# Kernel tuning notes

Measured on AMD Instinct MI355X. Metric: run time of the kernel, lower is better.

## Reference

```python
import jax, jax.numpy as jnp
import numpy as np

N_NODES = 1000000
N_EDGES = 32000000
NUM_GRAPHS = 1024


def setup_inputs() -> dict:
    key = jax.random.key(0)
    k1, k2, k3, k4, k5 = jax.random.split(key, 5)
    x = jax.random.normal(k1, (N_NODES, 1), dtype=jnp.float32)
    W = jax.random.normal(k2, (1, 1), dtype=jnp.float32)
    b = jax.random.normal(k3, (1,), dtype=jnp.float32)
    edge_index = jax.random.randint(k4, (2, N_EDGES), 0, N_NODES, dtype=jnp.int64)
    batch = jnp.sort(jax.random.randint(k5, (N_NODES,), 0, NUM_GRAPHS, dtype=jnp.int64))
    return {"x": x, "W": W, "b": b, "edge_index": edge_index, "batch": batch}


def reference(x, W, b, edge_index, batch):
    src, dst = edge_index[0], edge_index[1]
    # SimpleConv (default sum aggregation): out[i] = sum_{(j->i) in E} x[j]
    agg = jax.ops.segment_sum(x[src], dst, num_segments=N_NODES)  # [N,1]
    h = jax.nn.relu(agg)
    # global_mean_pool over graph ids
    sums = jax.ops.segment_sum(h, batch, num_segments=NUM_GRAPHS)  # [G,1]
    counts = jax.ops.segment_sum(jnp.ones((N_NODES,), dtype=h.dtype), batch,
                                 num_segments=NUM_GRAPHS)  # [G]
    pooled = sums / jnp.maximum(counts, 1.0)[:, None]
    # Linear(1 -> 1): y = pooled @ W^T + b
    return pooled @ W.T + b
```

## Files before the change

kernel.cpp:

```cpp
#include <hip/hip_runtime.h>

#define N_NODES    1000000
#define N_EDGES    32000000
#define NUM_GRAPHS 1024

typedef int          vint4  __attribute__((ext_vector_type(4)));
typedef unsigned int uint32;
typedef unsigned int vuint4 __attribute__((ext_vector_type(4)));

#define BUCKET_SHIFT 12
#define BUCKET_NODES (1 << BUCKET_SHIFT)
#define NBUCKETS     245

#define T1_NCHUNK   512
#define T1_BLOCK    512
#define T1_EDGES_PER_CHUNK (N_EDGES / T1_NCHUNK)
#define T1_QUADS    (T1_EDGES_PER_CHUNK / 4)
#define T1_QPR      (2 * T1_BLOCK)
#define T1_ROUNDS   ((T1_QUADS + T1_QPR - 1) / T1_QPR)
#define SCAP        64
#define SLAB_CAP    368

#define RSPLIT        4
#define CELLS_PER_WG  (T1_NCHUNK / RSPLIT)

#define T2_CAP      136192
#define T2_NCHUNK   512
#define T2_EPC      (N_EDGES / T2_NCHUNK)

#define GLDS(gp, lp) __builtin_amdgcn_global_load_lds(                         \
    (const __attribute__((address_space(1))) void*)(gp),                       \
    (__attribute__((address_space(3))) void*)(lp), 4, 0, 0)

__global__ __launch_bounds__(T1_BLOCK)
void slab_scatter(const int* __restrict__ src,
                  const int* __restrict__ dst,
                  uint32* __restrict__ slab,
                  uint32* __restrict__ fcnt_g,
                  uint32* __restrict__ ecnt_g) {
    __shared__ uint32 stage[NBUCKETS][SCAP];
    __shared__ uint32 rpos[NBUCKETS];
    __shared__ uint32 ecnt[NBUCKETS];
    __shared__ uint32 flushed[NBUCKETS];
    __shared__ uint32 carry[NBUCKETS];

    const int tid = threadIdx.x;
    const int w   = blockIdx.x;
    const vint4* d4 = (const vint4*)(dst + (size_t)w * T1_EDGES_PER_CHUNK);
    const vint4* s4 = (const vint4*)(src + (size_t)w * T1_EDGES_PER_CHUNK);

    for (int b = tid; b < NBUCKETS; b += T1_BLOCK) {
        rpos[b] = 0; ecnt[b] = 0; flushed[b] = 0; carry[b] = 0;
    }
    __syncthreads();

    const int grp    = tid >> 4;
    const int lane16 = tid & 15;

    for (int r = 0; r < T1_ROUNDS; ++r) {
        const int q0 = r * T1_QPR + tid;
        const int q1 = q0 + T1_BLOCK;
        const bool ok0 = q0 < T1_QUADS;
        const bool ok1 = q1 < T1_QUADS;
        vint4 d0, s0, d1, s1;
        if (ok0) { d0 = __builtin_nontemporal_load(&d4[q0]);
                   s0 = __builtin_nontemporal_load(&s4[q0]); }
        if (ok1) { d1 = __builtin_nontemporal_load(&d4[q1]);
                   s1 = __builtin_nontemporal_load(&s4[q1]); }

#define SCAT4(dd4, ss4)                                                        \
        {                                                                      \
            _Pragma("unroll")                                                  \
            for (int k = 0; k < 4; ++k) {                                      \
                uint32 dd = (uint32)(k == 0 ? dd4.x : k == 1 ? dd4.y :         \
                                     k == 2 ? dd4.z : dd4.w);                  \
                uint32 ss = (uint32)(k == 0 ? ss4.x : k == 1 ? ss4.y :         \
                                     k == 2 ? ss4.z : ss4.w);                  \
                uint32 b  = dd >> BUCKET_SHIFT;                                \
                uint32 v  = ((dd & (BUCKET_NODES - 1)) << 20) | ss;            \
                uint32 c  = carry[b] + atomicAdd(&rpos[b], 1u);                \
                if (c < SCAP) {                                                \
                    stage[b][c] = v;                                           \
                } else {                                                       \
                    uint32 e = atomicAdd(&ecnt[b], 1u);                        \
                    if (e < SLAB_CAP)          \
                        __builtin_nontemporal_store(v,                         \
                            &slab[((size_t)b * T1_NCHUNK + w) * SLAB_CAP       \
                                  + (SLAB_CAP - 1 - e)]);                      \
                }                                                              \
            }                                                                  \
        }
        if (ok0) SCAT4(d0, s0)
        if (ok1) SCAT4(d1, s1)
#undef SCAT4
        __syncthreads();
        for (int b = grp; b < NBUCKETS; b += 32) {
            uint32 tot = carry[b] + rpos[b];
            if (tot > SCAP) tot = SCAP;
            uint32 lines = tot >> 4;
            uint32 rem   = tot & 15u;
            uint32 fl    = flushed[b];
            uint32 maxl  = (SLAB_CAP > fl) ? ((SLAB_CAP - fl) >> 4) : 0u;
            if (lines > maxl) lines = maxl;
            uint32* dp = slab + ((size_t)b * T1_NCHUNK + w) * SLAB_CAP + fl;
            for (uint32 l = 0; l < lines; ++l)
                __builtin_nontemporal_store(stage[b][l * 16 + lane16],
                                            &dp[l * 16 + lane16]);
            if (lines) {
                uint32 mv = 0;
                if (lane16 < rem) mv = stage[b][lines * 16 + lane16];
                if (lane16 < rem) stage[b][lane16] = mv;
            }
            if (lane16 == 0) {
                flushed[b] = fl + lines * 16;
                carry[b]   = rem;
                rpos[b]    = 0;
            }
        }
        __syncthreads();
    }
    for (int b = grp; b < NBUCKETS; b += 32) {
        uint32 rem = carry[b];
        uint32 fl  = flushed[b];
        uint32* dp = slab + ((size_t)b * T1_NCHUNK + w) * SLAB_CAP + fl;
        if (lane16 < rem && fl + lane16 < SLAB_CAP)
            __builtin_nontemporal_store(stage[b][lane16], &dp[lane16]);
        if (lane16 == 0) {
            uint32 fc = fl + rem;
            fcnt_g[(size_t)b * T1_NCHUNK + w] = fc > SLAB_CAP ? SLAB_CAP : fc;
            ecnt_g[(size_t)b * T1_NCHUNK + w] = ecnt[b];
        }
    }
}

__global__ __launch_bounds__(1024)
void slab_reduce2(const uint32* __restrict__ slab,
                  const uint32* __restrict__ fcnt_g,
                  const uint32* __restrict__ ecnt_g,
                  const float* __restrict__ x,
                  float* __restrict__ agg) {
    __shared__ float  acc[BUCKET_NODES];
    __shared__ float  scr[16][8][64];
    __shared__ uint32 fc_s[CELLS_PER_WG];
    __shared__ uint32 ec_s[CELLS_PER_WG];

    const int b    = blockIdx.x / RSPLIT;
    const int part = blockIdx.x % RSPLIT;
    const int tid  = threadIdx.x;

    for (int n = tid; n < BUCKET_NODES; n += 1024) acc[n] = 0.0f;
    if (tid < CELLS_PER_WG) {
        size_t cell = (size_t)b * T1_NCHUNK + (size_t)part * CELLS_PER_WG + tid;
        uint32 fc = fcnt_g[cell];
        uint32 ec = ecnt_g[cell];
        if (fc > SLAB_CAP) fc = SLAB_CAP;
        if (ec > SLAB_CAP) ec = SLAB_CAP;
        fc_s[tid] = fc;
        ec_s[tid] = ec;
    }
    __syncthreads();

    const int wv = tid >> 6, lane = tid & 63;
    const size_t cbase = (size_t)b * T1_NCHUNK + (size_t)part * CELLS_PER_WG;

    for (int cp = wv; cp < CELLS_PER_WG; cp += 32) {
        const int cA = cp, cB = cp + 16;
        const uint32 fcA = fc_s[cA], fcB = fc_s[cB];
        const uint32 ecA = ec_s[cA], ecB = ec_s[cB];
        const uint32* baseA = slab + (cbase + cA) * SLAB_CAP;
        const uint32* baseB = slab + (cbase + cB) * SLAB_CAP;
        const uint32 nqA = fcA >> 2, nqB = fcB >> 2;
        const uint32 nqM = nqA > nqB ? nqA : nqB;

        for (uint32 i = lane; i < nqM; i += 64) {
            const bool aOK = i < nqA, bOK = i < nqB;
            vuint4 va = {0, 0, 0, 0}, vb = {0, 0, 0, 0};
            if (aOK) va = __builtin_nontemporal_load(&((const vuint4*)baseA)[i]);
            if (bOK) vb = __builtin_nontemporal_load(&((const vuint4*)baseB)[i]);
            GLDS(x + (va.x & 0xFFFFFu), &scr[wv][0][0]);
            GLDS(x + (va.y & 0xFFFFFu), &scr[wv][1][0]);
            GLDS(x + (va.z & 0xFFFFFu), &scr[wv][2][0]);
            GLDS(x + (va.w & 0xFFFFFu), &scr[wv][3][0]);
            GLDS(x + (vb.x & 0xFFFFFu), &scr[wv][4][0]);
            GLDS(x + (vb.y & 0xFFFFFu), &scr[wv][5][0]);
            GLDS(x + (vb.z & 0xFFFFFu), &scr[wv][6][0]);
            GLDS(x + (vb.w & 0xFFFFFu), &scr[wv][7][0]);
            asm volatile("s_waitcnt vmcnt(0)" ::: "memory");
            __builtin_amdgcn_sched_barrier(0);
            float a0 = scr[wv][0][lane], a1 = scr[wv][1][lane];
            float a2 = scr[wv][2][lane], a3 = scr[wv][3][lane];
            float b0 = scr[wv][4][lane], b1 = scr[wv][5][lane];
            float b2 = scr[wv][6][lane], b3 = scr[wv][7][lane];
            if (aOK) { atomicAdd(&acc[va.x >> 20], a0); atomicAdd(&acc[va.y >> 20], a1);
                       atomicAdd(&acc[va.z >> 20], a2); atomicAdd(&acc[va.w >> 20], a3); }
            if (bOK) { atomicAdd(&acc[vb.x >> 20], b0); atomicAdd(&acc[vb.y >> 20], b1);
                       atomicAdd(&acc[vb.z >> 20], b2); atomicAdd(&acc[vb.w >> 20], b3); }
            __builtin_amdgcn_sched_barrier(0);
        }
#define REM(base, fc, ec)                                                      \
        {                                                                      \
            for (uint32 i = ((fc) & ~3u) + lane; i < (fc); i += 64) {          \
                uint32 v = __builtin_nontemporal_load(&(base)[i]);             \
                atomicAdd(&acc[v >> 20], x[v & 0xFFFFFu]);                     \
            }                                                                  \
            for (uint32 i = lane; i < (ec); i += 64) {                         \
                uint32 v = (base)[SLAB_CAP - 1 - i];                           \
                atomicAdd(&acc[v >> 20], x[v & 0xFFFFFu]);                     \
            }                                                                  \
        }
        REM(baseA, fcA, ecA)
        REM(baseB, fcB, ecB)
#undef REM
    }
    __syncthreads();

    const int node0 = b << BUCKET_SHIFT;
    for (int n = tid; n < BUCKET_NODES; n += 1024) {
        float v = acc[n];
        if (v != 0.0f) atomicAdd(&agg[node0 + n], v);
    }
}

__global__ void finalize_kernel(const float* __restrict__ sums,
                                const float* __restrict__ counts,
                                const float* __restrict__ W,
                                const float* __restrict__ b,
                                float* __restrict__ out) {
    int g = blockIdx.x * blockDim.x + threadIdx.x;
    if (g < NUM_GRAPHS) {
        float pooled = sums[g] / fmaxf(counts[g], 1.0f);
        out[g] = pooled * W[0] + b[0];
    }
}

__global__ __launch_bounds__(1024)
void bucket_scatter(const int* __restrict__ src,
                    const int* __restrict__ dst,
                    uint32* __restrict__ sorted,
                    uint32* __restrict__ gpos) {
    __shared__ uint32 hist[NBUCKETS];
    __shared__ uint32 pos[NBUCKETS];
    const int tid = threadIdx.x;
    const size_t base = (size_t)blockIdx.x * T2_EPC;
    for (int b = tid; b < NBUCKETS; b += 1024) hist[b] = 0;
    __syncthreads();
    const vint4* d4 = (const vint4*)(dst + base);
    const vint4* s4 = (const vint4*)(src + base);
    const int nvec = T2_EPC / 4;
    for (int i = tid; i < nvec; i += 1024) {
        vint4 d = d4[i];
        atomicAdd(&hist[(uint32)d.x >> BUCKET_SHIFT], 1u);
        atomicAdd(&hist[(uint32)d.y >> BUCKET_SHIFT], 1u);
        atomicAdd(&hist[(uint32)d.z >> BUCKET_SHIFT], 1u);
        atomicAdd(&hist[(uint32)d.w >> BUCKET_SHIFT], 1u);
    }
    __syncthreads();
    for (int b = tid; b < NBUCKETS; b += 1024)
        pos[b] = atomicAdd(&gpos[b], hist[b]);
    __syncthreads();
    for (int i = tid; i < nvec; i += 1024) {
        vint4 d = d4[i];
        vint4 s = s4[i];
        #pragma unroll
        for (int k = 0; k < 4; ++k) {
            uint32 dd = (uint32)(k == 0 ? d.x : k == 1 ? d.y : k == 2 ? d.z : d.w);
            uint32 ss = (uint32)(k == 0 ? s.x : k == 1 ? s.y : k == 2 ? s.z : s.w);
            uint32 b = dd >> BUCKET_SHIFT, dl = dd & (BUCKET_NODES - 1);
            uint32 slot = atomicAdd(&pos[b], 1u);
            if (slot < T2_CAP) sorted[(size_t)b * T2_CAP + slot] = (dl << 20) | ss;
        }
    }
}

__global__ __launch_bounds__(1024)
void bucket_reduce(const uint32* __restrict__ sorted,
                   const uint32* __restrict__ gpos,
                   const float* __restrict__ x,
                   const int* __restrict__ batch,
                   float* __restrict__ sums,
                   float* __restrict__ counts) {
    __shared__ float acc[BUCKET_NODES];
    const int b = blockIdx.x;
    const int tid = threadIdx.x;
    for (int n = tid; n < BUCKET_NODES; n += 1024) acc[n] = 0.0f;
    __syncthreads();
    uint32 cnt = gpos[b];
    if (cnt > T2_CAP) cnt = T2_CAP;
    const uint32* reg = sorted + (size_t)b * T2_CAP;
    const vuint4* r4 = (const vuint4*)reg;
    const uint32 nvec = cnt / 4;
    for (uint32 i = tid; i < nvec; i += 1024) {
        vuint4 v = r4[i];
        atomicAdd(&acc[v.x >> 20], x[v.x & 0xFFFFFu]);
        atomicAdd(&acc[v.y >> 20], x[v.y & 0xFFFFFu]);
        atomicAdd(&acc[v.z >> 20], x[v.z & 0xFFFFFu]);
        atomicAdd(&acc[v.w >> 20], x[v.w & 0xFFFFFu]);
    }
    for (uint32 i = nvec * 4 + tid; i < cnt; i += 1024) {
        uint32 v = reg[i];
        atomicAdd(&acc[v >> 20], x[v & 0xFFFFFu]);
    }
    __syncthreads();
    const int node0 = b << BUCKET_SHIFT;
    for (int n = tid; n < BUCKET_NODES; n += 1024) {
        int i = node0 + n;
        float h = 0.0f;
        int g = -1;
        if (i < N_NODES) {
            h = fmaxf(acc[n], 0.0f);
            g = batch[i];
        }
        int g0 = __shfl(g, 0);
        if (__all(g == g0)) {
            #pragma unroll
            for (int off = 32; off > 0; off >>= 1)
                h += __shfl_down(h, off);
            if ((tid & 63) == 0 && g0 >= 0) {
                atomicAdd(&sums[g0], h);
                atomicAdd(&counts[g0], 64.0f);
            }
        } else if (g >= 0) {
            atomicAdd(&sums[g], h);
            atomicAdd(&counts[g], 1.0f);
        }
    }
}

__global__ void scatter_edges_dev(const vint4* __restrict__ src4,
                                  const vint4* __restrict__ dst4,
                                  const float* __restrict__ x,
                                  float* __restrict__ agg) {
    int t = blockIdx.x * blockDim.x + threadIdx.x;
    if (t < N_EDGES / 4) {
        vint4 s = __builtin_nontemporal_load(&src4[t]);
        vint4 d = __builtin_nontemporal_load(&dst4[t]);
        atomicAdd(&agg[d.x], x[s.x]);
        atomicAdd(&agg[d.y], x[s.y]);
        atomicAdd(&agg[d.z], x[s.z]);
        atomicAdd(&agg[d.w], x[s.w]);
    }
}

__global__ void pool_nodes_kernel(const float* __restrict__ agg,
                                  const int* __restrict__ batch,
                                  float* __restrict__ sums,
                                  float* __restrict__ counts) {
    int i = blockIdx.x * blockDim.x + threadIdx.x;
    float h = 0.0f;
    int g = -1;
    if (i < N_NODES) {
        h = fmaxf(agg[i], 0.0f);
        g = batch[i];
    }
    int g0 = __shfl(g, 0);
    if (__all(g == g0)) {
        #pragma unroll
        for (int off = 32; off > 0; off >>= 1)
            h += __shfl_down(h, off);
        if ((threadIdx.x & 63) == 0 && g0 >= 0) {
            atomicAdd(&sums[g0], h);
            atomicAdd(&counts[g0], 64.0f);
        }
    } else if (g >= 0) {
        atomicAdd(&sums[g], h);
        atomicAdd(&counts[g], 1.0f);
    }
}

extern "C" void kernel_launch(void* const* d_in, const int* in_sizes, int n_in,
                              void* d_out, int out_size, void* d_ws, size_t ws_size,
                              hipStream_t stream) {
    const float* x     = (const float*)d_in[0];
    const float* W     = (const float*)d_in[1];
    const float* b     = (const float*)d_in[2];
    const int*   edge  = (const int*)d_in[3];
    const int*   batch = (const int*)d_in[4];
    float* out = (float*)d_out;

    const int* src = edge;
    const int* dst = edge + N_EDGES;

    const size_t ncells     = (size_t)NBUCKETS * T1_NCHUNK;
    const size_t slab_elems = ncells * SLAB_CAP;
    const size_t nagg       = (size_t)NBUCKETS * BUCKET_NODES;
    const size_t need0 = (slab_elems + 2 * ncells + nagg + 2 * NUM_GRAPHS) * 4;
    const size_t t2_elems = (size_t)NBUCKETS * T2_CAP;
    const size_t need2 = (t2_elems + 256 + 2 * NUM_GRAPHS) * 4;

    if (ws_size >= need0) {
        uint32* slab   = (uint32*)d_ws;
        uint32* fcnt_g = slab + slab_elems;
        uint32* ecnt_g = fcnt_g + ncells;
        float*  agg    = (float*)(ecnt_g + ncells);
        float*  sums   = agg + nagg;
        float*  counts = sums + NUM_GRAPHS;
        (void)hipMemsetAsync(agg, 0, (nagg + 2 * NUM_GRAPHS) * 4, stream);

        slab_scatter<<<T1_NCHUNK, T1_BLOCK, 0, stream>>>(src, dst, slab, fcnt_g, ecnt_g);
        slab_reduce2<<<NBUCKETS * RSPLIT, 1024, 0, stream>>>(slab, fcnt_g, ecnt_g, x, agg);
        pool_nodes_kernel<<<(N_NODES + 255) / 256, 256, 0, stream>>>(agg, batch, sums, counts);
        finalize_kernel<<<(NUM_GRAPHS + 255) / 256, 256, 0, stream>>>(sums, counts, W, b, out);
    } else if (ws_size >= need2) {
        uint32* sorted = (uint32*)d_ws;
        uint32* gpos   = sorted + t2_elems;
        float*  sums   = (float*)(gpos + 256);
        float*  counts = sums + NUM_GRAPHS;
        (void)hipMemsetAsync(gpos, 0, (256 + 2 * NUM_GRAPHS) * 4, stream);

        bucket_scatter<<<T2_NCHUNK, 1024, 0, stream>>>(src, dst, sorted, gpos);
        bucket_reduce<<<NBUCKETS, 1024, 0, stream>>>(sorted, gpos, x, batch, sums, counts);
        finalize_kernel<<<(NUM_GRAPHS + 255) / 256, 256, 0, stream>>>(sums, counts, W, b, out);
    } else {
        float* agg    = (float*)d_ws;
        float* sums   = agg + N_NODES;
        float* counts = sums + NUM_GRAPHS;
        (void)hipMemsetAsync(d_ws, 0, ((size_t)N_NODES + 2 * NUM_GRAPHS) * 4, stream);

        int nthreads = N_EDGES / 4;
        scatter_edges_dev<<<(nthreads + 255) / 256, 256, 0, stream>>>(
            (const vint4*)src, (const vint4*)dst, x, agg);
        pool_nodes_kernel<<<(N_NODES + 255) / 256, 256, 0, stream>>>(agg, batch, sums, counts);
        finalize_kernel<<<(NUM_GRAPHS + 255) / 256, 256, 0, stream>>>(sums, counts, W, b, out);
    }
}
```

Measured before the change: 644.1 us.

## Gather source features during scatter and store value plus 16-bit local destination

Adds a new scatter/reduce path. The scatter kernel reads x[src] for each edge up front and writes two slabs: a float value and a 16-bit bucket-local destination. The reduce kernel then accumulates those values straight into LDS without gathering x. This moves the random x gather into the streaming pass and avoids a second indirect lookup. In exchange each slab entry grows from 4 to 6 bytes, the LDS staging depth per bucket is halved (more edges spill to the scattered overflow path), and the path needs a larger workspace to be taken.

```diff
diff --git a/kernel.cpp b/kernel.cpp
--- a/kernel.cpp
+++ b/kernel.cpp
@@ -4,9 +4,11 @@
 #define N_EDGES    32000000
 #define NUM_GRAPHS 1024
 
-typedef int          vint4  __attribute__((ext_vector_type(4)));
-typedef unsigned int uint32;
-typedef unsigned int vuint4 __attribute__((ext_vector_type(4)));
+typedef int            vint4    __attribute__((ext_vector_type(4)));
+typedef unsigned int   uint32;
+typedef unsigned int   vuint4   __attribute__((ext_vector_type(4)));
+typedef unsigned short vushort4 __attribute__((ext_vector_type(4)));
+typedef float          vfloat4  __attribute__((ext_vector_type(4)));
 
 #define BUCKET_SHIFT 12
 #define BUCKET_NODES (1 << BUCKET_SHIFT)
@@ -19,6 +21,7 @@
 #define T1_QPR      (2 * T1_BLOCK)
 #define T1_ROUNDS   ((T1_QUADS + T1_QPR - 1) / T1_QPR)
 #define SCAP        64
+#define SCAP_V      32
 #define SLAB_CAP    368
 
 #define RSPLIT        4
@@ -31,6 +34,193 @@
 #define GLDS(gp, lp) __builtin_amdgcn_global_load_lds(                         \
     (const __attribute__((address_space(1))) void*)(gp),                       \
     (__attribute__((address_space(3))) void*)(lp), 4, 0, 0)
+
+__global__ __launch_bounds__(T1_BLOCK)
+void slab_scatter_v(const int* __restrict__ src,
+                    const int* __restrict__ dst,
+                    const float* __restrict__ x,
+                    float*  __restrict__ vslab,
+                    unsigned short* __restrict__ dslab,
+                    uint32* __restrict__ fcnt_g,
+                    uint32* __restrict__ ecnt_g) {
+    __shared__ float          stage_v[NBUCKETS][SCAP_V];
+    __shared__ unsigned short stage_d[NBUCKETS][SCAP_V];
+    __shared__ uint32 rpos[NBUCKETS];
+    __shared__ uint32 ecnt[NBUCKETS];
+    __shared__ uint32 flushed[NBUCKETS];
+    __shared__ uint32 carry[NBUCKETS];
+
+    const int tid = threadIdx.x;
+    const int w   = blockIdx.x;
+    const vint4* d4 = (const vint4*)(dst + (size_t)w * T1_EDGES_PER_CHUNK);
+    const vint4* s4 = (const vint4*)(src + (size_t)w * T1_EDGES_PER_CHUNK);
+
+    for (int b = tid; b < NBUCKETS; b += T1_BLOCK) {
+        rpos[b] = 0; ecnt[b] = 0; flushed[b] = 0; carry[b] = 0;
+    }
+    __syncthreads();
+
+    const int grp    = tid >> 4;
+    const int lane16 = tid & 15;
+
+    for (int r = 0; r < T1_ROUNDS; ++r) {
+        const int q0 = r * T1_QPR + tid;
+        const int q1 = q0 + T1_BLOCK;
+        const bool ok0 = q0 < T1_QUADS;
+        const bool ok1 = q1 < T1_QUADS;
+        vint4 d0, s0, d1, s1;
+        if (ok0) { d0 = __builtin_nontemporal_load(&d4[q0]);
+                   s0 = __builtin_nontemporal_load(&s4[q0]); }
+        if (ok1) { d1 = __builtin_nontemporal_load(&d4[q1]);
+                   s1 = __builtin_nontemporal_load(&s4[q1]); }
+
+        float fv[8];
+        uint32 dv[8];
+        #pragma unroll
+        for (int k = 0; k < 8; ++k) {
+            const bool ok = (k < 4) ? ok0 : ok1;
+            if (ok) {
+                uint32 dd, ss;
+                if (k < 4) {
+                    dd = (uint32)(k == 0 ? d0.x : k == 1 ? d0.y : k == 2 ? d0.z : d0.w);
+                    ss = (uint32)(k == 0 ? s0.x : k == 1 ? s0.y : k == 2 ? s0.z : s0.w);
+                } else {
+                    dd = (uint32)(k == 4 ? d1.x : k == 5 ? d1.y : k == 6 ? d1.z : d1.w);
+                    ss = (uint32)(k == 4 ? s1.x : k == 5 ? s1.y : k == 6 ? s1.z : s1.w);
+                }
+                dv[k] = dd;
+                fv[k] = x[ss];
+            }
+        }
+        #pragma unroll
+        for (int k = 0; k < 8; ++k) {
+            const bool ok = (k < 4) ? ok0 : ok1;
+            if (ok) {
+                uint32 dd = dv[k];
+                uint32 b  = dd >> BUCKET_SHIFT;
+                uint32 dl = dd & (BUCKET_NODES - 1);
+                uint32 c  = carry[b] + atomicAdd(&rpos[b], 1u);
+                if (c < SCAP_V) {
+                    stage_v[b][c] = fv[k];
+                    stage_d[b][c] = (unsigned short)dl;
+                } else {
+                    uint32 e = atomicAdd(&ecnt[b], 1u);
+                    if (e < SLAB_CAP) {
+                        size_t idx = ((size_t)b * T1_NCHUNK + w) * SLAB_CAP
+                                     + (SLAB_CAP - 1 - e);
+                        __builtin_nontemporal_store(fv[k], &vslab[idx]);
+                        __builtin_nontemporal_store((unsigned short)dl, &dslab[idx]);
+                    }
+                }
+            }
+        }
+        __syncthreads();
+        for (int b = grp; b < NBUCKETS; b += 32) {
+            uint32 tot = carry[b] + rpos[b];
+            if (tot > SCAP_V) tot = SCAP_V;
+            uint32 lines = tot >> 4;
+            uint32 rem   = tot & 15u;
+            uint32 fl    = flushed[b];
+            uint32 maxl  = (SLAB_CAP > fl) ? ((SLAB_CAP - fl) >> 4) : 0u;
+            if (lines > maxl) lines = maxl;
+            size_t cbase = ((size_t)b * T1_NCHUNK + w) * SLAB_CAP + fl;
+            for (uint32 l = 0; l < lines; ++l) {
+                __builtin_nontemporal_store(stage_v[b][l * 16 + lane16],
+                                            &vslab[cbase + l * 16 + lane16]);
+                __builtin_nontemporal_store(stage_d[b][l * 16 + lane16],
+                                            &dslab[cbase + l * 16 + lane16]);
+            }
+            if (lines) {
+                float  mv = 0.0f; unsigned short md = 0;
+                if (lane16 < rem) { mv = stage_v[b][lines * 16 + lane16];
+                                    md = stage_d[b][lines * 16 + lane16]; }
+                if (lane16 < rem) { stage_v[b][lane16] = mv;
+                                    stage_d[b][lane16] = md; }
+            }
+            if (lane16 == 0) {
+                flushed[b] = fl + lines * 16;
+                carry[b]   = rem;
+                rpos[b]    = 0;
+            }
+        }
+        __syncthreads();
+    }
+    for (int b = grp; b < NBUCKETS; b += 32) {
+        uint32 rem = carry[b];
+        uint32 fl  = flushed[b];
+        size_t cbase = ((size_t)b * T1_NCHUNK + w) * SLAB_CAP + fl;
+        if (lane16 < rem && fl + lane16 < SLAB_CAP) {
+            __builtin_nontemporal_store(stage_v[b][lane16], &vslab[cbase + lane16]);
+            __builtin_nontemporal_store(stage_d[b][lane16], &dslab[cbase + lane16]);
+        }
+        if (lane16 == 0) {
+            uint32 fc = fl + rem;
+            fcnt_g[(size_t)b * T1_NCHUNK + w] = fc > SLAB_CAP ? SLAB_CAP : fc;
+            ecnt_g[(size_t)b * T1_NCHUNK + w] = ecnt[b];
+        }
+    }
+}
+
+__global__ __launch_bounds__(1024)
+void slab_reduce_v(const float* __restrict__ vslab,
+                   const unsigned short* __restrict__ dslab,
+                   const uint32* __restrict__ fcnt_g,
+                   const uint32* __restrict__ ecnt_g,
+                   float* __restrict__ agg) {
+    __shared__ float  acc[BUCKET_NODES];
+    __shared__ uint32 fc_s[CELLS_PER_WG];
+    __shared__ uint32 ec_s[CELLS_PER_WG];
+
+    const int b    = blockIdx.x / RSPLIT;
+    const int part = blockIdx.x % RSPLIT;
+    const int tid  = threadIdx.x;
+
+    for (int n = tid; n < BUCKET_NODES; n += 1024) acc[n] = 0.0f;
+    if (tid < CELLS_PER_WG) {
+        size_t cell = (size_t)b * T1_NCHUNK + (size_t)part * CELLS_PER_WG + tid;
+        uint32 fc = fcnt_g[cell];
+        uint32 ec = ecnt_g[cell];
+        if (fc > SLAB_CAP) fc = SLAB_CAP;
+        if (ec > SLAB_CAP) ec = SLAB_CAP;
+        fc_s[tid] = fc;
+        ec_s[tid] = ec;
+    }
+    __syncthreads();
+
+    const int wv = tid >> 6, lane = tid & 63;
+    const size_t cbase0 = (size_t)b * T1_NCHUNK + (size_t)part * CELLS_PER_WG;
+
+    for (int c = wv; c < CELLS_PER_WG; c += 16) {
+        const size_t cb = (cbase0 + c) * SLAB_CAP;
+        const uint32 fc = fc_s[c];
+        const uint32 ec = ec_s[c];
+        const uint32 nq = fc >> 2;
+        const vfloat4*  v4 = (const vfloat4*)(vslab + cb);
+        const vushort4* d4 = (const vushort4*)(dslab + cb);
+        for (uint32 i = lane; i < nq; i += 64) {
+            vfloat4  v = __builtin_nontemporal_load(&v4[i]);
+            vushort4 d = __builtin_nontemporal_load(&d4[i]);
+            atomicAdd(&acc[d.x], v.x);
+            atomicAdd(&acc[d.y], v.y);
+            atomicAdd(&acc[d.z], v.z);
+            atomicAdd(&acc[d.w], v.w);
+        }
+        for (uint32 i = (fc & ~3u) + lane; i < fc; i += 64) {
+            atomicAdd(&acc[dslab[cb + i]], vslab[cb + i]);
+        }
+        for (uint32 i = lane; i < ec; i += 64) {
+            size_t idx = cb + SLAB_CAP - 1 - i;
+            atomicAdd(&acc[dslab[idx]], vslab[idx]);
+        }
+    }
+    __syncthreads();
+
+    const int node0 = b << BUCKET_SHIFT;
+    for (int n = tid; n < BUCKET_NODES; n += 1024) {
+        float v = acc[n];
+        if (v != 0.0f) atomicAdd(&agg[node0 + n], v);
+    }
+}
 
 __global__ __launch_bounds__(T1_BLOCK)
 void slab_scatter(const int* __restrict__ src,
@@ -83,7 +273,7 @@
                     stage[b][c] = v;                                           \
                 } else {                                                       \
                     uint32 e = atomicAdd(&ecnt[b], 1u);                        \
-                    if (e < SLAB_CAP)          \
+                    if (e < SLAB_CAP)                                          \
                         __builtin_nontemporal_store(v,                         \
                             &slab[((size_t)b * T1_NCHUNK + w) * SLAB_CAP       \
                                   + (SLAB_CAP - 1 - e)]);                      \
@@ -383,11 +573,30 @@
     const size_t ncells     = (size_t)NBUCKETS * T1_NCHUNK;
     const size_t slab_elems = ncells * SLAB_CAP;
     const size_t nagg       = (size_t)NBUCKETS * BUCKET_NODES;
-    const size_t need0 = (slab_elems + 2 * ncells + nagg + 2 * NUM_GRAPHS) * 4;
+
+    const size_t needv = slab_elems * 4 + slab_elems * 2
+                       + ncells * 4 * 2 + nagg * 4 + 2 * NUM_GRAPHS * 4;
+    const size_t need1 = (slab_elems + 2 * ncells + nagg + 2 * NUM_GRAPHS) * 4;
     const size_t t2_elems = (size_t)NBUCKETS * T2_CAP;
     const size_t need2 = (t2_elems + 256 + 2 * NUM_GRAPHS) * 4;
 
-    if (ws_size >= need0) {
+    if (ws_size >= needv) {
+        float*          vslab  = (float*)d_ws;
+        unsigned short* dslab  = (unsigned short*)(vslab + slab_elems);
+        uint32*         fcnt_g = (uint32*)(dslab + slab_elems);
+        uint32*         ecnt_g = fcnt_g + ncells;
+        float*          agg    = (float*)(ecnt_g + ncells);
+        float*          sums   = agg + nagg;
+        float*          counts = sums + NUM_GRAPHS;
+        (void)hipMemsetAsync(agg, 0, (nagg + 2 * NUM_GRAPHS) * 4, stream);
+
+        slab_scatter_v<<<T1_NCHUNK, T1_BLOCK, 0, stream>>>(
+            src, dst, x, vslab, dslab, fcnt_g, ecnt_g);
+        slab_reduce_v<<<NBUCKETS * RSPLIT, 1024, 0, stream>>>(
+            vslab, dslab, fcnt_g, ecnt_g, agg);
+        pool_nodes_kernel<<<(N_NODES + 255) / 256, 256, 0, stream>>>(agg, batch, sums, counts);
+        finalize_kernel<<<(NUM_GRAPHS + 255) / 256, 256, 0, stream>>>(sums, counts, W, b, out);
+    } else if (ws_size >= need1) {
         uint32* slab   = (uint32*)d_ws;
         uint32* fcnt_g = slab + slab_elems;
         uint32* ecnt_g = fcnt_g + ncells;
```

Measured after the change: 872.9 us. 1.36x slower.
